# Optimization experiments

Measured on AMD Instinct MI355X. Metric: run time of the kernel, lower is better.

Reference implementation:

```python
import jax, jax.numpy as jnp
import numpy as np

H = 8   # num_heads
D = 64  # out_features per head

def setup_inputs() -> dict:
    key = jax.random.key(0)
    k1, k2, k3, k4 = jax.random.split(key, 4)
    B, N, F_IN, E = 2, 8192, 512, 65536
    x = jax.random.normal(k1, (B, N, F_IN), dtype=jnp.float32)
    edge_indices = jax.random.randint(k2, (2, E), 0, N)
    W = jax.random.normal(k3, (H * D, F_IN), dtype=jnp.float32) * (1.0 / np.sqrt(F_IN))
    a = jax.random.normal(k4, (2 * D, 1), dtype=jnp.float32) * 0.1
    return {"x": x, "edge_indices": edge_indices, "W": W, "a": a}

def reference(x, edge_indices, W, a):
    # Faithful translation of GraphAttentionLayer.forward (eval mode: dropout = identity).
    B, N, _ = x.shape
    h = (x @ W.T).reshape(B, N, H, D)              # [B,N,H,D]
    src, dst = edge_indices[0], edge_indices[1]
    E = src.shape[0]
    h_src = h[:, src]                               # [B,E,H,D]
    h_dst = h[:, dst]                               # [B,E,H,D]
    # cat([h_src,h_dst]) @ a  ==  h_src @ a[:D] + h_dst @ a[D:]
    a1, a2 = a[:D, 0], a[D:, 0]
    scores = jnp.einsum('behd,d->beh', h_src, a1) + jnp.einsum('behd,d->beh', h_dst, a2)
    scores = jax.nn.leaky_relu(scores, negative_slope=0.2)      # [B,E,H]
    # NOTE: original code softmaxes over the BATCH dim (dim=0) per edge.
    sm = jax.nn.softmax(scores, axis=0)                          # [B,E,H]
    last_edge = jnp.full((N,), -1, dtype=jnp.int32).at[src].max(
        jnp.arange(E, dtype=jnp.int32))                          # [N]
    has_edge = last_edge >= 0
    w = jnp.where(has_edge[None, :, None],
                  sm[:, jnp.clip(last_edge, 0)], 0.0)            # [B,N,H]
    # aggregated[:, s] += w[:, s, :, None] * h_dst[:, e] for each edge e with src[e]==s
    # (weights fully built before aggregation loop) => w[s] * segment_sum(h_dst over src)
    agg_dst = jnp.zeros((B, N, H, D), dtype=h.dtype).at[:, src].add(h_dst)
    aggregated = w[..., None] * agg_dst                          # [B,N,H,D]
    return aggregated.mean(axis=2)                               # [B,N,D]
```

## Files before the change

kernel.cpp:

```cpp
#include <hip/hip_runtime.h>
#include <stdint.h>

#define H_HEADS 8
#define DDIM 64
#define NNODES 8192
#define BB 2
#define FIN 512
#define FOUT 512
#define EDGES 65536
#define CAP 32

typedef unsigned short u16;
typedef unsigned int u32;
typedef __bf16 bf16x8 __attribute__((ext_vector_type(8)));
typedef float f32x4 __attribute__((ext_vector_type(4)));

__device__ __forceinline__ u16 f2bf(float f) {
    u32 u = __float_as_uint(f);
    return (u16)((u + 0x7FFFu + ((u >> 16) & 1u)) >> 16);
}
__device__ __forceinline__ float bf2f(u32 s) {
    return __uint_as_float(s << 16);
}
__device__ __forceinline__ uint4 pack8(float4 a, float4 b) {
    return make_uint4(f2bf(a.x) | ((u32)f2bf(a.y) << 16),
                      f2bf(a.z) | ((u32)f2bf(a.w) << 16),
                      f2bf(b.x) | ((u32)f2bf(b.y) << 16),
                      f2bf(b.z) | ((u32)f2bf(b.w) << 16));
}

#define NWB (FOUT * FIN / 8 / 256)
#define NEB 64
__global__ __launch_bounds__(256) void prep_kernel(
    const float* __restrict__ W, const int* __restrict__ src,
    const int* __restrict__ dst, u16* __restrict__ Wb,
    int* __restrict__ cursor, int* __restrict__ last_edge,
    int* __restrict__ csr_dst) {
    int blk = blockIdx.x;
    if (blk < NWB) {
        int i = blk * 256 + threadIdx.x;
        const float4* p = (const float4*)W;
        float4 v0 = p[(size_t)i * 2], v1 = p[(size_t)i * 2 + 1];
        ((uint4*)Wb)[i] = pack8(v0, v1);
    } else {
        int t = (blk - NWB) * 256 + threadIdx.x;
#pragma unroll
        for (int k = 0; k < 4; k++) {
            int e = t * 4 + k;
            int s = src[e], d = dst[e];
            int slot = atomicAdd(&cursor[s], 1);
            if (slot < CAP) csr_dst[(size_t)s * CAP + slot] = d;
            atomicMax(&last_edge[s], e);
        }
    }
}

#define GLDS(g, l)                                                              \
    __builtin_amdgcn_global_load_lds(                                           \
        (const __attribute__((address_space(1))) u32*)(g),                      \
        (__attribute__((address_space(3))) u32*)(l), 16, 0, 0)

__global__ __launch_bounds__(256) void gemm_mfma(const float* __restrict__ X,
                                                 const u16* __restrict__ Bm,
                                                 const float* __restrict__ a,
                                                 u16* __restrict__ C,
                                                 float* __restrict__ s1,
                                                 float* __restrict__ s2) {
    __shared__ u16 As[128 * 32];
    __shared__ u16 Bs[128 * 32];
    int tid = threadIdx.x;
    int m0 = blockIdx.y * 128, n0 = blockIdx.x * 128;
    int lane = tid & 63, wv = tid >> 6;
    int wr = (wv >> 1) * 64, wc = (wv & 1) * 64;
    int l15 = lane & 15, quad = lane >> 4;
    f32x4 acc[4][4] = {};

    float a1v[4], a2v[4];
#pragma unroll
    for (int j = 0; j < 4; j++) {
        a1v[j] = a[j * 16 + l15];
        a2v[j] = a[DDIM + j * 16 + l15];
    }

    int srow = tid >> 2;
    int scol = (tid & 3) * 8;
    const float* Ag = X + (size_t)(m0 + srow) * FIN + scol;
    const u16* Bg = Bm + (size_t)(n0 + srow) * FIN + scol;
    u16* Al = As + tid * 8;
    u16* Bl = Bs + tid * 8;

    for (int k0 = 0; k0 < FIN; k0 += 32) {
        __syncthreads();
        GLDS(Bg + k0, Bl);
        GLDS(Bg + k0 + (size_t)64 * FIN, Bl + 64 * 32);
        float4 fa0 = *(const float4*)(Ag + k0);
        float4 fa1 = *(const float4*)(Ag + k0 + 4);
        float4 fb0 = *(const float4*)(Ag + k0 + (size_t)64 * FIN);
        float4 fb1 = *(const float4*)(Ag + k0 + (size_t)64 * FIN + 4);
        *(uint4*)Al = pack8(fa0, fa1);
        *(uint4*)(Al + 64 * 32) = pack8(fb0, fb1);
        __syncthreads();
        bf16x8 af[4], bfr[4];
#pragma unroll
        for (int i = 0; i < 4; i++)
            af[i] = *(const bf16x8*)(As + (wr + i * 16 + l15) * 32 + quad * 8);
#pragma unroll
        for (int j = 0; j < 4; j++)
            bfr[j] = *(const bf16x8*)(Bs + (wc + j * 16 + l15) * 32 + quad * 8);
#pragma unroll
        for (int i = 0; i < 4; i++)
#pragma unroll
            for (int j = 0; j < 4; j++)
                acc[i][j] = __builtin_amdgcn_mfma_f32_16x16x32_bf16(
                    af[i], bfr[j], acc[i][j], 0, 0, 0);
    }

#pragma unroll
    for (int i = 0; i < 4; i++) {
        int row_base = m0 + wr + i * 16 + quad * 4;
#pragma unroll
        for (int j = 0; j < 4; j++) {
            int col = n0 + wc + j * 16 + l15;
#pragma unroll
            for (int r = 0; r < 4; r++)
                C[(size_t)(row_base + r) * FOUT + col] = f2bf(acc[i][j][r]);
        }
    }

    int head = blockIdx.x * 2 + (wv & 1);
#pragma unroll
    for (int i = 0; i < 4; i++) {
#pragma unroll
        for (int r = 0; r < 4; r++) {
            float p1 = 0.f, p2 = 0.f;
#pragma unroll
            for (int j = 0; j < 4; j++) {
                p1 += a1v[j] * acc[i][j][r];
                p2 += a2v[j] * acc[i][j][r];
            }
#pragma unroll
            for (int m = 1; m <= 8; m <<= 1) {
                p1 += __shfl_xor(p1, m);
                p2 += __shfl_xor(p2, m);
            }
            if (l15 == 0) {
                int row = m0 + wr + i * 16 + quad * 4 + r;
                s1[row * H_HEADS + head] = p1;
                s2[row * H_HEADS + head] = p2;
            }
        }
    }
}

__global__ __launch_bounds__(256) void aggregate(const u16* __restrict__ h,
                                                 const float* __restrict__ s1,
                                                 const float* __restrict__ s2,
                                                 const int* __restrict__ cursor,
                                                 const int* __restrict__ last_edge,
                                                 const int* __restrict__ dst,
                                                 const int* __restrict__ csr_dst,
                                                 float* __restrict__ out, int N) {
    int n = blockIdx.x * 2 + (threadIdx.x >> 7);
    int b = (threadIdx.x >> 6) & 1;
    int lane = threadIdx.x & 63;
    int head = lane >> 3;

    int deg = cursor[n];
    deg = deg < CAP ? deg : CAP;

    float wgt = 0.f;
    if (deg > 0) {
        int dl = dst[last_edge[n]];
        float sc0 = s1[(0 * N + n) * H_HEADS + head] +
                    s2[((size_t)0 * N + dl) * H_HEADS + head];
        float sc1 = s1[((size_t)1 * N + n) * H_HEADS + head] +
                    s2[((size_t)1 * N + dl) * H_HEADS + head];
        sc0 = sc0 >= 0.f ? sc0 : 0.2f * sc0;
        sc1 = sc1 >= 0.f ? sc1 : 0.2f * sc1;
        float m = fmaxf(sc0, sc1);
        float e0 = __expf(sc0 - m), e1 = __expf(sc1 - m);
        wgt = (b == 0 ? e0 : e1) / (e0 + e1);
    }

    const int* cp = csr_dst + (size_t)n * CAP;
    int myidx = (lane < CAP) ? cp[lane] : 0;

    float acc[8] = {};
    const u16* hb = h + (size_t)b * N * FOUT + lane * 8;
    for (int j0 = 0; j0 < deg; j0 += 4) {
#pragma unroll
        for (int k = 0; k < 4; k++) {
            int j = j0 + k;
            float f = (j < deg) ? 1.0f : 0.0f;
            int dn = (j < deg) ? __shfl(myidx, j) : 0;
            uint4 v = *(const uint4*)(hb + (size_t)dn * FOUT);
            acc[0] = fmaf(f, bf2f(v.x & 0xffffu), acc[0]);
            acc[1] = fmaf(f, bf2f(v.x >> 16), acc[1]);
            acc[2] = fmaf(f, bf2f(v.y & 0xffffu), acc[2]);
            acc[3] = fmaf(f, bf2f(v.y >> 16), acc[3]);
            acc[4] = fmaf(f, bf2f(v.z & 0xffffu), acc[4]);
            acc[5] = fmaf(f, bf2f(v.z >> 16), acc[5]);
            acc[6] = fmaf(f, bf2f(v.w & 0xffffu), acc[6]);
            acc[7] = fmaf(f, bf2f(v.w >> 16), acc[7]);
        }
    }
    float val[8];
#pragma unroll
    for (int k = 0; k < 8; k++) val[k] = acc[k] * wgt;
#pragma unroll
    for (int m = 8; m <= 32; m <<= 1)
#pragma unroll
        for (int k = 0; k < 8; k++) val[k] += __shfl_xor(val[k], m);
    if (lane < 8) {
        float* op = out + ((size_t)b * N + n) * DDIM + lane * 8;
        const float inv = 1.0f / H_HEADS;
        *(float4*)op = make_float4(val[0] * inv, val[1] * inv, val[2] * inv,
                                   val[3] * inv);
        *(float4*)(op + 4) = make_float4(val[4] * inv, val[5] * inv,
                                         val[6] * inv, val[7] * inv);
    }
}

extern "C" void kernel_launch(void* const* d_in, const int* in_sizes, int n_in,
                              void* d_out, int out_size, void* d_ws,
                              size_t ws_size, hipStream_t stream) {
    const float* x = (const float*)d_in[0];
    const int* edges = (const int*)d_in[1];
    const float* W = (const float*)d_in[2];
    const float* a = (const float*)d_in[3];
    float* out = (float*)d_out;

    const int* src = edges;
    const int* dst = edges + EDGES;

    char* p = (char*)d_ws;
    auto carve = [&](size_t bytes) {
        char* r = p;
        p += (bytes + 255) & ~(size_t)255;
        return r;
    };
    u16* Wb = (u16*)carve((size_t)FOUT * FIN * 2);
    u16* h = (u16*)carve((size_t)BB * NNODES * FOUT * 2);
    float* s1 = (float*)carve((size_t)BB * NNODES * H_HEADS * 4);
    float* s2 = (float*)carve((size_t)BB * NNODES * H_HEADS * 4);
    int* cursor = (int*)carve(NNODES * 4);
    int* last_edge = (int*)carve(NNODES * 4);
    int* csr_dst = (int*)carve((size_t)NNODES * CAP * 4);

    const int M = BB * NNODES;

    hipMemsetAsync(cursor, 0, 2 * NNODES * 4, stream);
    prep_kernel<<<NWB + NEB, 256, 0, stream>>>(W, src, dst, Wb, cursor,
                                               last_edge, csr_dst);
    gemm_mfma<<<dim3(FOUT / 128, M / 128), 256, 0, stream>>>(x, Wb, a, h, s1,
                                                             s2);
    aggregate<<<NNODES / 2, 256, 0, stream>>>(h, s1, s2, cursor, last_edge, dst,
                                              csr_dst, out, NNODES);
}
```

Before: 131.1 us.

## Fold CSR build into GEMM launch with LDS atomics and packed last-edge

Removes the memset and moves the edge bucketing out of the W-conversion kernel into 64 extra blocks of the GEMM grid. Each of those blocks scans all edges and keeps only the sources in its 128-node range, using LDS atomics instead of global ones. The last edge and its dst are packed into one int so that aggregate skips an indirect dst load. The cost is that each bucketing block reads the full edge list. CSR slot order also becomes nondeterministic in a different way, which is fine for a sum.

```diff
diff --git a/kernel.cpp b/kernel.cpp
--- a/kernel.cpp
+++ b/kernel.cpp
@@ -9,6 +9,7 @@
 #define FOUT 512
 #define EDGES 65536
 #define CAP 32
+#define NEBLK 64
 
 typedef unsigned short u16;
 typedef unsigned int u32;
@@ -29,30 +30,12 @@
                       f2bf(b.z) | ((u32)f2bf(b.w) << 16));
 }
 
-#define NWB (FOUT * FIN / 8 / 256)
-#define NEB 64
-__global__ __launch_bounds__(256) void prep_kernel(
-    const float* __restrict__ W, const int* __restrict__ src,
-    const int* __restrict__ dst, u16* __restrict__ Wb,
-    int* __restrict__ cursor, int* __restrict__ last_edge,
-    int* __restrict__ csr_dst) {
-    int blk = blockIdx.x;
-    if (blk < NWB) {
-        int i = blk * 256 + threadIdx.x;
-        const float4* p = (const float4*)W;
-        float4 v0 = p[(size_t)i * 2], v1 = p[(size_t)i * 2 + 1];
-        ((uint4*)Wb)[i] = pack8(v0, v1);
-    } else {
-        int t = (blk - NWB) * 256 + threadIdx.x;
-#pragma unroll
-        for (int k = 0; k < 4; k++) {
-            int e = t * 4 + k;
-            int s = src[e], d = dst[e];
-            int slot = atomicAdd(&cursor[s], 1);
-            if (slot < CAP) csr_dst[(size_t)s * CAP + slot] = d;
-            atomicMax(&last_edge[s], e);
-        }
-    }
+__global__ __launch_bounds__(256) void prep_w(const float* __restrict__ W,
+                                              u16* __restrict__ Wb) {
+    int i = blockIdx.x * 256 + threadIdx.x;
+    const float4* p = (const float4*)W;
+    float4 v0 = p[(size_t)i * 2], v1 = p[(size_t)i * 2 + 1];
+    ((uint4*)Wb)[i] = pack8(v0, v1);
 }
 
 #define GLDS(g, l)                                                              \
@@ -60,16 +43,44 @@
         (const __attribute__((address_space(1))) u32*)(g),                      \
         (__attribute__((address_space(3))) u32*)(l), 16, 0, 0)
 
-__global__ __launch_bounds__(256) void gemm_mfma(const float* __restrict__ X,
-                                                 const u16* __restrict__ Bm,
-                                                 const float* __restrict__ a,
-                                                 u16* __restrict__ C,
-                                                 float* __restrict__ s1,
-                                                 float* __restrict__ s2) {
+__global__ __launch_bounds__(256) void gemm_mfma(
+    const float* __restrict__ X, const u16* __restrict__ Bm,
+    const float* __restrict__ a, const int* __restrict__ src,
+    const int* __restrict__ dst, u16* __restrict__ C, float* __restrict__ s1,
+    float* __restrict__ s2, int* __restrict__ cursor,
+    int* __restrict__ le_pack, int* __restrict__ csr_dst) {
     __shared__ u16 As[128 * 32];
     __shared__ u16 Bs[128 * 32];
     int tid = threadIdx.x;
-    int m0 = blockIdx.y * 128, n0 = blockIdx.x * 128;
+    int blk = blockIdx.x;
+
+    if (blk < NEBLK) {
+        int base = blk * 128;
+        int* cnt = (int*)As;
+        int* lastp = cnt + 128;
+        if (tid < 128) { cnt[tid] = 0; lastp[tid] = -1; }
+        __syncthreads();
+        for (int c = 0; c < EDGES; c += 256) {
+            int e = c + tid;
+            int s = src[e];
+            unsigned r = (unsigned)(s - base);
+            if (r < 128u) {
+                int d = dst[e];
+                int slot = atomicAdd(&cnt[r], 1);
+                if (slot < CAP) csr_dst[(size_t)s * CAP + slot] = d;
+                atomicMax(&lastp[r], (e << 13) | d);
+            }
+        }
+        __syncthreads();
+        if (tid < 128) {
+            cursor[base + tid] = cnt[tid];
+            le_pack[base + tid] = lastp[tid];
+        }
+        return;
+    }
+
+    int gb = blk - NEBLK;
+    int m0 = (gb >> 2) * 128, n0 = (gb & 3) * 128;
     int lane = tid & 63, wv = tid >> 6;
     int wr = (wv >> 1) * 64, wc = (wv & 1) * 64;
     int l15 = lane & 15, quad = lane >> 4;
@@ -127,7 +138,7 @@
         }
     }
 
-    int head = blockIdx.x * 2 + (wv & 1);
+    int head = (gb & 3) * 2 + (wv & 1);
 #pragma unroll
     for (int i = 0; i < 4; i++) {
 #pragma unroll
@@ -156,8 +167,7 @@
                                                  const float* __restrict__ s1,
                                                  const float* __restrict__ s2,
                                                  const int* __restrict__ cursor,
-                                                 const int* __restrict__ last_edge,
-                                                 const int* __restrict__ dst,
+                                                 const int* __restrict__ le_pack,
                                                  const int* __restrict__ csr_dst,
                                                  float* __restrict__ out, int N) {
     int n = blockIdx.x * 2 + (threadIdx.x >> 7);
@@ -167,10 +177,14 @@
 
     int deg = cursor[n];
     deg = deg < CAP ? deg : CAP;
+    int pk = le_pack[n];
+
+    const int* cp = csr_dst + (size_t)n * CAP;
+    int myidx = (lane < CAP) ? cp[lane] : 0;
 
     float wgt = 0.f;
-    if (deg > 0) {
-        int dl = dst[last_edge[n]];
+    if (pk >= 0) {
+        int dl = pk & 8191;
         float sc0 = s1[(0 * N + n) * H_HEADS + head] +
                     s2[((size_t)0 * N + dl) * H_HEADS + head];
         float sc1 = s1[((size_t)1 * N + n) * H_HEADS + head] +
@@ -181,9 +195,6 @@
         float e0 = __expf(sc0 - m), e1 = __expf(sc1 - m);
         wgt = (b == 0 ? e0 : e1) / (e0 + e1);
     }
-
-    const int* cp = csr_dst + (size_t)n * CAP;
-    int myidx = (lane < CAP) ? cp[lane] : 0;
 
     float acc[8] = {};
     const u16* hb = h + (size_t)b * N * FOUT + lane * 8;
@@ -244,16 +255,14 @@
     float* s1 = (float*)carve((size_t)BB * NNODES * H_HEADS * 4);
     float* s2 = (float*)carve((size_t)BB * NNODES * H_HEADS * 4);
     int* cursor = (int*)carve(NNODES * 4);
-    int* last_edge = (int*)carve(NNODES * 4);
+    int* le_pack = (int*)carve(NNODES * 4);
     int* csr_dst = (int*)carve((size_t)NNODES * CAP * 4);
 
     const int M = BB * NNODES;
 
-    hipMemsetAsync(cursor, 0, 2 * NNODES * 4, stream);
-    prep_kernel<<<NWB + NEB, 256, 0, stream>>>(W, src, dst, Wb, cursor,
-                                               last_edge, csr_dst);
-    gemm_mfma<<<dim3(FOUT / 128, M / 128), 256, 0, stream>>>(x, Wb, a, h, s1,
-                                                             s2);
-    aggregate<<<NNODES / 2, 256, 0, stream>>>(h, s1, s2, cursor, last_edge, dst,
+    prep_w<<<FOUT * FIN / 8 / 256, 256, 0, stream>>>(W, Wb);
+    gemm_mfma<<<NEBLK + (M / 128) * (FOUT / 128), 256, 0, stream>>>(
+        x, Wb, a, src, dst, h, s1, s2, cursor, le_pack, csr_dst);
+    aggregate<<<NNODES / 2, 256, 0, stream>>>(h, s1, s2, cursor, le_pack,
                                               csr_dst, out, NNODES);
 }
```

Result: slower. 195.7 us (+49.2%).
